# Performance work log

Measured on AMD Instinct MI355X. Metric: run time of the kernel, lower is better.

The kernel has to match this reference:

```python
import jax, jax.numpy as jnp
import numpy as np

D = 768
EPS = 1e-5

def _layernorm(x, g, b):
    mu = jnp.mean(x, axis=-1, keepdims=True)
    var = jnp.mean(jnp.square(x - mu), axis=-1, keepdims=True)
    return (x - mu) * jax.lax.rsqrt(var + EPS) * g + b

def setup_inputs() -> dict:
    key = jax.random.key(0)
    ks = jax.random.split(key, 12)
    s = 1.0 / np.sqrt(D)
    x = jax.random.normal(ks[0], (8, 2048, D), dtype=jnp.float32)
    Wq = jax.random.uniform(ks[1], (D, D), jnp.float32, -s, s)
    bq = jax.random.uniform(ks[2], (D,), jnp.float32, -s, s)
    Wk = jax.random.uniform(ks[3], (D, D), jnp.float32, -s, s)
    bk = jax.random.uniform(ks[4], (D,), jnp.float32, -s, s)
    Wv = jax.random.uniform(ks[5], (D, D), jnp.float32, -s, s)
    bv = jax.random.uniform(ks[6], (D,), jnp.float32, -s, s)
    W1 = jax.random.uniform(ks[7], (D, D), jnp.float32, -s, s)
    b1 = jax.random.uniform(ks[8], (D,), jnp.float32, -s, s)
    W2 = jax.random.uniform(ks[9], (D, D), jnp.float32, -s, s)
    b2 = jax.random.uniform(ks[10], (D,), jnp.float32, -s, s)
    g_n1 = jnp.ones((D,), jnp.float32); be_n1 = jnp.zeros((D,), jnp.float32)
    g_n2 = jnp.ones((D,), jnp.float32); be_n2 = jnp.zeros((D,), jnp.float32)
    return {"x": x, "Wq": Wq, "bq": bq, "Wk": Wk, "bk": bk, "Wv": Wv, "bv": bv,
            "W1": W1, "b1": b1, "W2": W2, "b2": b2,
            "g_n1": g_n1, "be_n1": be_n1, "g_n2": g_n2, "be_n2": be_n2}

def reference(x, Wq, bq, Wk, bk, Wv, bv, W1, b1, W2, b2, g_n1, be_n1, g_n2, be_n2):
    # pre-norm single-head self-attention (scores materialized as in source)
    h = _layernorm(x, g_n1, be_n1)
    q = h @ Wq.T + bq  # [B,S,D]
    k = h @ Wk.T + bk
    v = h @ Wv.T + bv
    scores = jnp.einsum('bsd,btd->bst', q, k) / jnp.sqrt(jnp.float32(D))
    attn = jax.nn.softmax(scores, axis=-1)
    x = jnp.einsum('bst,btd->bsd', attn, v) + x
    # MLP: two Linear(d,d) each followed by exact GELU (matches source MLP)
    h = _layernorm(x, g_n2, be_n2)
    h = jax.nn.gelu(h @ W1.T + b1, approximate=False)
    h = jax.nn.gelu(h @ W2.T + b2, approximate=False)
    return h + x
```

## Files before the change

kernel.cpp:

```cpp
#include <hip/hip_runtime.h>
#include <cstdint>
#include <cstddef>

#define D_MODEL 768
#define NBATCH 8
#define SEQLEN 2048
#define NROWS (NBATCH*SEQLEN)

typedef __attribute__((ext_vector_type(4))) float  f32x4;
typedef __attribute__((ext_vector_type(8))) __bf16 bf16x8;
typedef __attribute__((ext_vector_type(4))) __bf16 bf16x4;
typedef __attribute__((ext_vector_type(8))) _Float16 f16x8;

#define MFMA16(a,b,c) __builtin_amdgcn_mfma_f32_16x16x32_bf16(a,b,c,0,0,0)
#define SCALE 0.03608439182435161f
#define AS1 __attribute__((address_space(1)))
#define AS3 __attribute__((address_space(3)))

static constexpr size_t SZ_ACT = (size_t)NROWS * D_MODEL * 2;
static constexpr size_t OFF_Q    = 0;
static constexpr size_t OFF_K    = OFF_Q + SZ_ACT;
static constexpr size_t OFF_VT   = OFF_K + SZ_ACT;
static constexpr size_t OFF_X2   = OFF_VT + SZ_ACT;
static constexpr size_t OFF_W    = OFF_X2 + (size_t)NROWS*D_MODEL*4;
static constexpr size_t OFF_POOL = OFF_W + (size_t)5*589824*2;

__device__ __forceinline__ float gelu_exact(float x) {
  return 0.5f * x * (1.0f + erff(x * 0.70710678118654752f));
}

__device__ __forceinline__ int xcd_remap(int p, int chunk) {
  return (p & 7) * chunk + (p >> 3);
}

__global__ __launch_bounds__(256) void k_cvt5(
    const float* __restrict__ s0, const float* __restrict__ s1,
    const float* __restrict__ s2, const float* __restrict__ s3,
    const float* __restrict__ s4, __bf16* __restrict__ dst)
{
  const int wsel = blockIdx.y;
  const float* s = wsel==0 ? s0 : wsel==1 ? s1 : wsel==2 ? s2 : wsel==3 ? s3 : s4;
  const size_t i = ((size_t)blockIdx.x*256 + threadIdx.x)*4;
  float4 v = *(const float4*)(s + i);
  bf16x4 o;
  o[0] = (__bf16)v.x; o[1] = (__bf16)v.y; o[2] = (__bf16)v.z; o[3] = (__bf16)v.w;
  *(bf16x4*)(dst + (size_t)wsel*589824 + i) = o;
}

__global__ __launch_bounds__(256) void k_layernorm(
    const float* __restrict__ x, const float* __restrict__ g,
    const float* __restrict__ be, __bf16* __restrict__ out)
{
  const int row  = blockIdx.x*4 + (threadIdx.x>>6);
  const int lane = threadIdx.x & 63;
  const float4* xr = (const float4*)(x + (size_t)row*D_MODEL);
  float4 v[3];
  float s = 0.f, ss = 0.f;
#pragma unroll
  for (int j=0;j<3;j++){
    v[j] = xr[lane + 64*j];
    s  += v[j].x + v[j].y + v[j].z + v[j].w;
    ss += v[j].x*v[j].x + v[j].y*v[j].y + v[j].z*v[j].z + v[j].w*v[j].w;
  }
#pragma unroll
  for (int d=1; d<64; d<<=1){ s += __shfl_xor(s,d); ss += __shfl_xor(ss,d); }
  const float mu   = s  * (1.f/768.f);
  const float var  = ss * (1.f/768.f) - mu*mu;
  const float rstd = rsqrtf(var + 1e-5f);
  __bf16* orow = out + (size_t)row*D_MODEL;
#pragma unroll
  for (int j=0;j<3;j++){
    const int c0 = (lane + 64*j)*4;
    bf16x4 o;
    o[0] = (__bf16)((v[j].x - mu)*rstd*g[c0+0] + be[c0+0]);
    o[1] = (__bf16)((v[j].y - mu)*rstd*g[c0+1] + be[c0+1]);
    o[2] = (__bf16)((v[j].z - mu)*rstd*g[c0+2] + be[c0+2]);
    o[3] = (__bf16)((v[j].w - mu)*rstd*g[c0+3] + be[c0+3]);
    *(bf16x4*)(orow + c0) = o;
  }
}

__global__ __launch_bounds__(256) void k_transpose_v(
    const __bf16* __restrict__ v, __bf16* __restrict__ vT)
{
  __shared__ __bf16 tile[64][72];
  const int b = blockIdx.z;
  const int t0 = blockIdx.x*64, d0 = blockIdx.y*64;
  const int tid = threadIdx.x;
  const int rr = (tid>>3)*2, cc = (tid&7)*8;
  const __bf16* src = v + ((size_t)b*SEQLEN + t0)*D_MODEL + d0;
#pragma unroll
  for (int j=0;j<2;j++){
    bf16x8 val = *(const bf16x8*)(src + (size_t)(rr+j)*D_MODEL + cc);
#pragma unroll
    for (int e=0;e<8;e++) tile[cc+e][rr+j] = val[e];
  }
  __syncthreads();
  __bf16* dst = vT + ((size_t)b*D_MODEL + d0)*SEQLEN + t0;
#pragma unroll
  for (int j=0;j<2;j++){
    bf16x8 o;
#pragma unroll
    for (int e=0;e<8;e++) o[e] = tile[rr+j][cc+e];
    *(bf16x8*)(dst + (size_t)(rr+j)*SEQLEN + cc) = o;
  }
}

__global__ __launch_bounds__(256) void k_softmax(_Float16* __restrict__ S)
{
  const int row  = blockIdx.x*4 + (threadIdx.x>>6);
  const int lane = threadIdx.x & 63;
  _Float16* sr = S + (size_t)row*SEQLEN + lane*32;
  f16x8 v[4];
#pragma unroll
  for (int j=0;j<4;j++) v[j] = *(const f16x8*)(sr + j*8);
  float f[32];
  float mx = -1e30f;
#pragma unroll
  for (int j=0;j<4;j++)
#pragma unroll
    for (int e=0;e<8;e++){ f[j*8+e] = (float)v[j][e]; mx = fmaxf(mx, f[j*8+e]); }
#pragma unroll
  for (int d=1; d<64; d<<=1) mx = fmaxf(mx, __shfl_xor(mx, d));
  float sum = 0.f;
#pragma unroll
  for (int i=0;i<32;i++){ f[i] = __expf(f[i]-mx); sum += f[i]; }
#pragma unroll
  for (int d=1; d<64; d<<=1) sum += __shfl_xor(sum, d);
  const float inv = 1.f/sum;
  __bf16* pr = (__bf16*)(S + (size_t)row*SEQLEN) + lane*32;
#pragma unroll
  for (int j=0;j<4;j++){
    bf16x8 o;
#pragma unroll
    for (int e=0;e<8;e++) o[e] = (__bf16)(f[j*8+e]*inv);
    *(bf16x8*)(pr + j*8) = o;
  }
}

template<int NT>
__device__ __forceinline__ void gemm_core_d2(
    const __bf16* __restrict__ Asrc, const int ldA,
    const __bf16* __restrict__ Bsrc, const int ldB,
    f32x4 (&acc)[4][4])
{
  __shared__ __bf16 As[2*4096];
  __shared__ __bf16 Bs[2*4096];
  const int tid = threadIdx.x, w = tid>>6, lane = tid&63;
  const int wr = w>>1, wc = w&1, l16 = lane&15, l4 = lane>>4;
  const int rs  = (l16 ^ (l16>>2)) & 3;
  const int rdo = (l4 ^ rs) * 8;
  const int srl = lane>>2;
  const int ssw = (((lane&3) ^ ((srl ^ (srl>>2)) & 3))) * 8;

#pragma unroll
  for (int mi=0;mi<4;mi++)
#pragma unroll
    for (int ni=0;ni<4;ni++)
      acc[mi][ni] = (f32x4){0.f,0.f,0.f,0.f};

#define STG2(T_) { \
    const int kb_ = (T_)*32; \
    const int sb_ = ((T_)&1)*4096; \
    _Pragma("unroll") \
    for (int i_=0;i_<2;i_++){ \
      const int ii_ = w + i_*4; \
      const int rl_ = ii_*16 + srl; \
      __builtin_amdgcn_global_load_lds((const AS1 void*)(Asrc + (size_t)rl_*ldA + kb_ + ssw), (AS3 void*)(As + sb_ + ii_*512), 16, 0, 0); \
      __builtin_amdgcn_global_load_lds((const AS1 void*)(Bsrc + (size_t)rl_*ldB + kb_ + ssw), (AS3 void*)(Bs + sb_ + ii_*512), 16, 0, 0); \
    } }

  STG2(0) STG2(1)

  for (int t=0; t<NT; ++t){
    if (t+1 < NT) asm volatile("s_waitcnt vmcnt(4)" ::: "memory");
    else          asm volatile("s_waitcnt vmcnt(0)" ::: "memory");
    __builtin_amdgcn_s_barrier();
    const int sb = (t&1)*4096;
    bf16x8 af[4], bq[4];
#pragma unroll
    for (int mi=0;mi<4;mi++)
      af[mi] = *(const bf16x8*)(As + sb + (wr*64 + mi*16 + l16)*32 + rdo);
#pragma unroll
    for (int ni=0;ni<4;ni++)
      bq[ni] = *(const bf16x8*)(Bs + sb + (wc*64 + ni*16 + l16)*32 + rdo);
    asm volatile("s_waitcnt lgkmcnt(0)" ::: "memory");
    __builtin_amdgcn_sched_barrier(0);
    __builtin_amdgcn_s_barrier();
    if (t+2 < NT) STG2(t+2)
    __builtin_amdgcn_s_setprio(1);
#pragma unroll
    for (int mi=0;mi<4;mi++)
#pragma unroll
      for (int ni=0;ni<4;ni++)
        acc[mi][ni] = MFMA16(af[mi], bq[ni], acc[mi][ni]);
    __builtin_amdgcn_s_setprio(0);
  }
#undef STG2
}

__global__ __launch_bounds__(256) void k_qkv(
    const __bf16* __restrict__ A, const __bf16* __restrict__ W,
    const float* __restrict__ bq, const float* __restrict__ bk, const float* __restrict__ bv,
    __bf16* __restrict__ Cq, __bf16* __restrict__ Ck, __bf16* __restrict__ Cv)
{
  const int L = xcd_remap(blockIdx.x, 288);
  const int bm = L/18, bn = L%18;
  f32x4 acc[4][4];
  gemm_core_d2<24>(A + (size_t)bm*128*D_MODEL, D_MODEL, W + (size_t)bn*128*D_MODEL, D_MODEL, acc);
  const int tid = threadIdx.x, w=tid>>6, lane=tid&63;
  const int wr=w>>1, wc=w&1, l16=lane&15, l4=lane>>4;
  const int seg = bn/6;
  const int colb = (bn%6)*128 + wc*64;
  const float* bias = seg==0?bq:(seg==1?bk:bv);
  __bf16* C = seg==0?Cq:(seg==1?Ck:Cv);
  const int row0 = bm*128 + wr*64;
#pragma unroll
  for (int ni=0;ni<4;ni++){
    const int col = colb + ni*16 + l16;
    const float bb = bias[col];
#pragma unroll
    for (int mi=0;mi<4;mi++)
#pragma unroll
      for (int r=0;r<4;r++){
        const int row = row0 + mi*16 + l4*4 + r;
        float v = acc[mi][ni][r] + bb;
        if (seg==0) v *= SCALE;
        C[(size_t)row*D_MODEL + col] = (__bf16)v;
      }
  }
}

__global__ __launch_bounds__(256) void k_s(
    const __bf16* __restrict__ Q, const __bf16* __restrict__ K, _Float16* __restrict__ S,
    int chunk)
{
  const int L = xcd_remap(blockIdx.x, chunk);
  const int batch = L>>8, r = L&255;
  const int bm = r>>4, bn = r&15;
  const size_t bo = (size_t)batch * SEQLEN * D_MODEL;
  f32x4 acc[4][4];
  gemm_core_d2<24>(Q + bo + (size_t)bm*128*D_MODEL, D_MODEL, K + bo + (size_t)bn*128*D_MODEL, D_MODEL, acc);
  const int tid = threadIdx.x, w=tid>>6, lane=tid&63;
  const int wr=w>>1, wc=w&1, l16=lane&15, l4=lane>>4;
  _Float16* Sb = S + (size_t)batch*SEQLEN*SEQLEN;
  const int row0 = bm*128 + wr*64, col0 = bn*128 + wc*64;
#pragma unroll
  for (int ni=0;ni<4;ni++){
    const int col = col0 + ni*16 + l16;
#pragma unroll
    for (int mi=0;mi<4;mi++)
#pragma unroll
      for (int r2=0;r2<4;r2++)
        Sb[(size_t)(row0 + mi*16 + l4*4 + r2)*SEQLEN + col] = (_Float16)acc[mi][ni][r2];
  }
}

__global__ __launch_bounds__(256) void k_pv(
    const __bf16* __restrict__ P, const __bf16* __restrict__ VT,
    const float* __restrict__ x, float* __restrict__ x2, int bbase, int chunk)
{
  const int L = xcd_remap(blockIdx.x, chunk);
  const int by = L/96, r = L%96;
  const int bm = r/6, bn = r%6;
  const int bidx = bbase + by;
  f32x4 acc[4][4];
  gemm_core_d2<64>(P + (size_t)by*SEQLEN*SEQLEN + (size_t)bm*128*SEQLEN, SEQLEN,
                   VT + (size_t)bidx*D_MODEL*SEQLEN + (size_t)bn*128*SEQLEN, SEQLEN, acc);
  const int tid = threadIdx.x, w=tid>>6, lane=tid&63;
  const int wr=w>>1, wc=w&1, l16=lane&15, l4=lane>>4;
  const size_t row0 = (size_t)bidx*SEQLEN + bm*128 + wr*64;
  const int col0 = bn*128 + wc*64;
#pragma unroll
  for (int ni=0;ni<4;ni++){
    const int col = col0 + ni*16 + l16;
#pragma unroll
    for (int mi=0;mi<4;mi++)
#pragma unroll
      for (int r2=0;r2<4;r2++){
        const size_t row = row0 + mi*16 + l4*4 + r2;
        x2[row*D_MODEL + col] = acc[mi][ni][r2] + x[row*D_MODEL + col];
      }
  }
}

template<int RES>
__global__ __launch_bounds__(256) void k_mlp(
    const __bf16* __restrict__ A, const __bf16* __restrict__ W,
    const float* __restrict__ bias, const float* __restrict__ resid, void* __restrict__ out)
{
  const int L = xcd_remap(blockIdx.x, 96);
  const int bm = L/6, bn = L%6;
  f32x4 acc[4][4];
  gemm_core_d2<24>(A + (size_t)bm*128*D_MODEL, D_MODEL, W + (size_t)bn*128*D_MODEL, D_MODEL, acc);
  const int tid = threadIdx.x, w=tid>>6, lane=tid&63;
  const int wr=w>>1, wc=w&1, l16=lane&15, l4=lane>>4;
  const int row0 = bm*128 + wr*64, col0 = bn*128 + wc*64;
#pragma unroll
  for (int ni=0;ni<4;ni++){
    const int col = col0 + ni*16 + l16;
    const float bb = bias[col];
#pragma unroll
    for (int mi=0;mi<4;mi++)
#pragma unroll
      for (int r=0;r<4;r++){
        const int row = row0 + mi*16 + l4*4 + r;
        float v = gelu_exact(acc[mi][ni][r] + bb);
        if (RES) ((float*)out)[(size_t)row*D_MODEL + col] = v + resid[(size_t)row*D_MODEL + col];
        else     ((__bf16*)out)[(size_t)row*D_MODEL + col] = (__bf16)v;
      }
  }
}

extern "C" void kernel_launch(void* const* d_in, const int* in_sizes, int n_in,
                              void* d_out, int out_size, void* d_ws, size_t ws_size,
                              hipStream_t stream)
{
  const float* x   = (const float*)d_in[0];
  const float* Wq  = (const float*)d_in[1];
  const float* bq  = (const float*)d_in[2];
  const float* Wk  = (const float*)d_in[3];
  const float* bk  = (const float*)d_in[4];
  const float* Wv  = (const float*)d_in[5];
  const float* bv  = (const float*)d_in[6];
  const float* W1  = (const float*)d_in[7];
  const float* b1  = (const float*)d_in[8];
  const float* W2  = (const float*)d_in[9];
  const float* b2  = (const float*)d_in[10];
  const float* g1  = (const float*)d_in[11];
  const float* be1 = (const float*)d_in[12];
  const float* g2  = (const float*)d_in[13];
  const float* be2 = (const float*)d_in[14];
  (void)in_sizes; (void)n_in; (void)out_size;

  char* ws = (char*)d_ws;
  __bf16*   qb  = (__bf16*)(ws + OFF_Q);
  __bf16*   kb  = (__bf16*)(ws + OFF_K);
  __bf16*   vT  = (__bf16*)(ws + OFF_VT);
  float*    x2  = (float*)(ws + OFF_X2);
  __bf16*   wbf = (__bf16*)(ws + OFF_W);
  __bf16*   h1  = (__bf16*)(ws + OFF_POOL);
  __bf16*   vb  = (__bf16*)(ws + OFF_POOL + SZ_ACT);
  _Float16* Sp  = (_Float16*)(ws + OFF_POOL);
  __bf16*   h2  = h1;
  __bf16*   h3  = qb;

  const bool big = ws_size >= OFF_POOL + (size_t)NBATCH*SEQLEN*SEQLEN*2;

  k_cvt5<<<dim3(576,5,1),256,0,stream>>>(Wq,Wk,Wv,W1,W2,wbf);
  k_layernorm<<<dim3(4096),256,0,stream>>>(x, g1, be1, h1);
  k_qkv<<<dim3(2304),256,0,stream>>>(h1, wbf, bq, bk, bv, qb, kb, vb);
  k_transpose_v<<<dim3(32,12,8),256,0,stream>>>(vb, vT);

  if (big){
    k_s<<<dim3(2048),256,0,stream>>>(qb, kb, Sp, 256);
    k_softmax<<<dim3(4096),256,0,stream>>>(Sp);
    k_pv<<<dim3(768),256,0,stream>>>((const __bf16*)Sp, vT, x, x2, 0, 96);
  } else {
    for (int c=0;c<2;c++){
      const size_t qoff = (size_t)c*4*SEQLEN*D_MODEL;
      k_s<<<dim3(1024),256,0,stream>>>(qb + qoff, kb + qoff, Sp, 128);
      k_softmax<<<dim3(2048),256,0,stream>>>(Sp);
      k_pv<<<dim3(384),256,0,stream>>>((const __bf16*)Sp, vT, x, x2, c*4, 48);
    }
  }

  k_layernorm<<<dim3(4096),256,0,stream>>>(x2, g2, be2, h2);
  k_mlp<0><<<dim3(768),256,0,stream>>>(h2, wbf + (size_t)3*589824, b1, nullptr, h3);
  k_mlp<1><<<dim3(768),256,0,stream>>>(h3, wbf + (size_t)4*589824, b2, x2, d_out);
}
```

Before: 393.6 us.

## Fuse V transpose into QKV epilogue and change GEMM LDS swizzle layout

Removes the separate V transpose kernel and its intermediate buffer: the QKV GEMM epilogue now writes V directly in transposed layout using 4-element vector stores along the sequence dimension. The shared GEMM core also gets a new LDS staging/read swizzle that packs two rows per 64-element line, meant to reduce bank conflicts on fragment reads. This saves one launch plus a full read and write of V, but the transposed epilogue stores are strided by SEQLEN, and the new swizzle changes every GEMM's access pattern.

```diff
diff --git a/kernel.cpp b/kernel.cpp
--- a/kernel.cpp
+++ b/kernel.cpp
@@ -80,32 +80,6 @@
   }
 }
 
-__global__ __launch_bounds__(256) void k_transpose_v(
-    const __bf16* __restrict__ v, __bf16* __restrict__ vT)
-{
-  __shared__ __bf16 tile[64][72];
-  const int b = blockIdx.z;
-  const int t0 = blockIdx.x*64, d0 = blockIdx.y*64;
-  const int tid = threadIdx.x;
-  const int rr = (tid>>3)*2, cc = (tid&7)*8;
-  const __bf16* src = v + ((size_t)b*SEQLEN + t0)*D_MODEL + d0;
-#pragma unroll
-  for (int j=0;j<2;j++){
-    bf16x8 val = *(const bf16x8*)(src + (size_t)(rr+j)*D_MODEL + cc);
-#pragma unroll
-    for (int e=0;e<8;e++) tile[cc+e][rr+j] = val[e];
-  }
-  __syncthreads();
-  __bf16* dst = vT + ((size_t)b*D_MODEL + d0)*SEQLEN + t0;
-#pragma unroll
-  for (int j=0;j<2;j++){
-    bf16x8 o;
-#pragma unroll
-    for (int e=0;e<8;e++) o[e] = tile[rr+j][cc+e];
-    *(bf16x8*)(dst + (size_t)(rr+j)*SEQLEN + cc) = o;
-  }
-}
-
 __global__ __launch_bounds__(256) void k_softmax(_Float16* __restrict__ S)
 {
   const int row  = blockIdx.x*4 + (threadIdx.x>>6);
@@ -139,7 +113,7 @@
 }
 
 template<int NT>
-__device__ __forceinline__ void gemm_core_d2(
+__device__ __forceinline__ void gemm_core_rp(
     const __bf16* __restrict__ Asrc, const int ldA,
     const __bf16* __restrict__ Bsrc, const int ldB,
     f32x4 (&acc)[4][4])
@@ -148,10 +122,16 @@
   __shared__ __bf16 Bs[2*4096];
   const int tid = threadIdx.x, w = tid>>6, lane = tid&63;
   const int wr = w>>1, wc = w&1, l16 = lane&15, l4 = lane>>4;
-  const int rs  = (l16 ^ (l16>>2)) & 3;
-  const int rdo = (l4 ^ rs) * 8;
-  const int srl = lane>>2;
-  const int ssw = (((lane&3) ^ ((srl ^ (srl>>2)) & 3))) * 8;
+
+  const int rql   = l16>>1;
+  const int rslot = (((l16&1)<<2) + l4) ^ rql;
+  const int roff  = rql*64 + rslot*8;
+
+  const int su  = (lane&7) ^ (lane>>3);
+  const int ss_ = (su>>2)&1;
+  const int sg_ = su&3;
+  const int srw = 2*(lane>>3) + ss_;
+  const int sco = sg_*8;
 
 #pragma unroll
   for (int mi=0;mi<4;mi++)
@@ -159,18 +139,18 @@
     for (int ni=0;ni<4;ni++)
       acc[mi][ni] = (f32x4){0.f,0.f,0.f,0.f};
 
-#define STG2(T_) { \
+#define STGRP(T_) { \
     const int kb_ = (T_)*32; \
     const int sb_ = ((T_)&1)*4096; \
     _Pragma("unroll") \
     for (int i_=0;i_<2;i_++){ \
       const int ii_ = w + i_*4; \
-      const int rl_ = ii_*16 + srl; \
-      __builtin_amdgcn_global_load_lds((const AS1 void*)(Asrc + (size_t)rl_*ldA + kb_ + ssw), (AS3 void*)(As + sb_ + ii_*512), 16, 0, 0); \
-      __builtin_amdgcn_global_load_lds((const AS1 void*)(Bsrc + (size_t)rl_*ldB + kb_ + ssw), (AS3 void*)(Bs + sb_ + ii_*512), 16, 0, 0); \
+      const int rg_ = ii_*16 + srw; \
+      __builtin_amdgcn_global_load_lds((const AS1 void*)(Asrc + (size_t)rg_*ldA + kb_ + sco), (AS3 void*)(As + sb_ + ii_*512), 16, 0, 0); \
+      __builtin_amdgcn_global_load_lds((const AS1 void*)(Bsrc + (size_t)rg_*ldB + kb_ + sco), (AS3 void*)(Bs + sb_ + ii_*512), 16, 0, 0); \
     } }
 
-  STG2(0) STG2(1)
+  STGRP(0) STGRP(1)
 
   for (int t=0; t<NT; ++t){
     if (t+1 < NT) asm volatile("s_waitcnt vmcnt(4)" ::: "memory");
@@ -180,14 +160,14 @@
     bf16x8 af[4], bq[4];
 #pragma unroll
     for (int mi=0;mi<4;mi++)
-      af[mi] = *(const bf16x8*)(As + sb + (wr*64 + mi*16 + l16)*32 + rdo);
+      af[mi] = *(const bf16x8*)(As + sb + (wr*32 + mi*8)*64 + roff);
 #pragma unroll
     for (int ni=0;ni<4;ni++)
-      bq[ni] = *(const bf16x8*)(Bs + sb + (wc*64 + ni*16 + l16)*32 + rdo);
+      bq[ni] = *(const bf16x8*)(Bs + sb + (wc*32 + ni*8)*64 + roff);
     asm volatile("s_waitcnt lgkmcnt(0)" ::: "memory");
     __builtin_amdgcn_sched_barrier(0);
     __builtin_amdgcn_s_barrier();
-    if (t+2 < NT) STG2(t+2)
+    if (t+2 < NT) STGRP(t+2)
     __builtin_amdgcn_s_setprio(1);
 #pragma unroll
     for (int mi=0;mi<4;mi++)
@@ -196,38 +176,56 @@
         acc[mi][ni] = MFMA16(af[mi], bq[ni], acc[mi][ni]);
     __builtin_amdgcn_s_setprio(0);
   }
-#undef STG2
+#undef STGRP
 }
 
 __global__ __launch_bounds__(256) void k_qkv(
     const __bf16* __restrict__ A, const __bf16* __restrict__ W,
     const float* __restrict__ bq, const float* __restrict__ bk, const float* __restrict__ bv,
-    __bf16* __restrict__ Cq, __bf16* __restrict__ Ck, __bf16* __restrict__ Cv)
+    __bf16* __restrict__ Cq, __bf16* __restrict__ Ck, __bf16* __restrict__ vT)
 {
   const int L = xcd_remap(blockIdx.x, 288);
   const int bm = L/18, bn = L%18;
   f32x4 acc[4][4];
-  gemm_core_d2<24>(A + (size_t)bm*128*D_MODEL, D_MODEL, W + (size_t)bn*128*D_MODEL, D_MODEL, acc);
+  gemm_core_rp<24>(A + (size_t)bm*128*D_MODEL, D_MODEL, W + (size_t)bn*128*D_MODEL, D_MODEL, acc);
   const int tid = threadIdx.x, w=tid>>6, lane=tid&63;
   const int wr=w>>1, wc=w&1, l16=lane&15, l4=lane>>4;
   const int seg = bn/6;
   const int colb = (bn%6)*128 + wc*64;
-  const float* bias = seg==0?bq:(seg==1?bk:bv);
-  __bf16* C = seg==0?Cq:(seg==1?Ck:Cv);
   const int row0 = bm*128 + wr*64;
-#pragma unroll
-  for (int ni=0;ni<4;ni++){
-    const int col = colb + ni*16 + l16;
-    const float bb = bias[col];
-#pragma unroll
-    for (int mi=0;mi<4;mi++)
-#pragma unroll
-      for (int r=0;r<4;r++){
-        const int row = row0 + mi*16 + l4*4 + r;
-        float v = acc[mi][ni][r] + bb;
-        if (seg==0) v *= SCALE;
-        C[(size_t)row*D_MODEL + col] = (__bf16)v;
+  if (seg < 2){
+    const float* bias = seg==0 ? bq : bk;
+    __bf16* C = seg==0 ? Cq : Ck;
+#pragma unroll
+    for (int ni=0;ni<4;ni++){
+      const int col = colb + ni*16 + l16;
+      const float bb = bias[col];
+#pragma unroll
+      for (int mi=0;mi<4;mi++)
+#pragma unroll
+        for (int r=0;r<4;r++){
+          const int row = row0 + mi*16 + l4*4 + r;
+          float v = acc[mi][ni][r] + bb;
+          if (seg==0) v *= SCALE;
+          C[(size_t)row*D_MODEL + col] = (__bf16)v;
+        }
+    }
+  } else {
+    const int b = row0 >> 11;
+    const int trow0 = row0 & 2047;
+    __bf16* vtb = vT + (size_t)b*D_MODEL*SEQLEN;
+#pragma unroll
+    for (int ni=0;ni<4;ni++){
+      const int col = colb + ni*16 + l16;
+      const float bb = bv[col];
+#pragma unroll
+      for (int mi=0;mi<4;mi++){
+        bf16x4 o;
+#pragma unroll
+        for (int r=0;r<4;r++) o[r] = (__bf16)(acc[mi][ni][r] + bb);
+        *(bf16x4*)(vtb + (size_t)col*SEQLEN + trow0 + mi*16 + l4*4) = o;
       }
+    }
   }
 }
 
@@ -240,7 +238,7 @@
   const int bm = r>>4, bn = r&15;
   const size_t bo = (size_t)batch * SEQLEN * D_MODEL;
   f32x4 acc[4][4];
-  gemm_core_d2<24>(Q + bo + (size_t)bm*128*D_MODEL, D_MODEL, K + bo + (size_t)bn*128*D_MODEL, D_MODEL, acc);
+  gemm_core_rp<24>(Q + bo + (size_t)bm*128*D_MODEL, D_MODEL, K + bo + (size_t)bn*128*D_MODEL, D_MODEL, acc);
   const int tid = threadIdx.x, w=tid>>6, lane=tid&63;
   const int wr=w>>1, wc=w&1, l16=lane&15, l4=lane>>4;
   _Float16* Sb = S + (size_t)batch*SEQLEN*SEQLEN;
@@ -265,7 +263,7 @@
   const int bm = r/6, bn = r%6;
   const int bidx = bbase + by;
   f32x4 acc[4][4];
-  gemm_core_d2<64>(P + (size_t)by*SEQLEN*SEQLEN + (size_t)bm*128*SEQLEN, SEQLEN,
+  gemm_core_rp<64>(P + (size_t)by*SEQLEN*SEQLEN + (size_t)bm*128*SEQLEN, SEQLEN,
                    VT + (size_t)bidx*D_MODEL*SEQLEN + (size_t)bn*128*SEQLEN, SEQLEN, acc);
   const int tid = threadIdx.x, w=tid>>6, lane=tid&63;
   const int wr=w>>1, wc=w&1, l16=lane&15, l4=lane>>4;
@@ -292,7 +290,7 @@
   const int L = xcd_remap(blockIdx.x, 96);
   const int bm = L/6, bn = L%6;
   f32x4 acc[4][4];
-  gemm_core_d2<24>(A + (size_t)bm*128*D_MODEL, D_MODEL, W + (size_t)bn*128*D_MODEL, D_MODEL, acc);
+  gemm_core_rp<24>(A + (size_t)bm*128*D_MODEL, D_MODEL, W + (size_t)bn*128*D_MODEL, D_MODEL, acc);
   const int tid = threadIdx.x, w=tid>>6, lane=tid&63;
   const int wr=w>>1, wc=w&1, l16=lane&15, l4=lane>>4;
   const int row0 = bm*128 + wr*64, col0 = bn*128 + wc*64;
@@ -340,7 +338,6 @@
   float*    x2  = (float*)(ws + OFF_X2);
   __bf16*   wbf = (__bf16*)(ws + OFF_W);
   __bf16*   h1  = (__bf16*)(ws + OFF_POOL);
-  __bf16*   vb  = (__bf16*)(ws + OFF_POOL + SZ_ACT);
   _Float16* Sp  = (_Float16*)(ws + OFF_POOL);
   __bf16*   h2  = h1;
   __bf16*   h3  = qb;
@@ -349,8 +346,7 @@
 
   k_cvt5<<<dim3(576,5,1),256,0,stream>>>(Wq,Wk,Wv,W1,W2,wbf);
   k_layernorm<<<dim3(4096),256,0,stream>>>(x, g1, be1, h1);
-  k_qkv<<<dim3(2304),256,0,stream>>>(h1, wbf, bq, bk, bv, qb, kb, vb);
-  k_transpose_v<<<dim3(32,12,8),256,0,stream>>>(vb, vT);
+  k_qkv<<<dim3(2304),256,0,stream>>>(h1, wbf, bq, bk, bv, qb, kb, vT);
 
   if (big){
     k_s<<<dim3(2048),256,0,stream>>>(qb, kb, Sp, 256);
```

Result: faster. 384.7 us (-2.3%).
